# Optimization experiments

Measured on AMD Instinct MI355X. Metric: run time of the kernel, lower is better.

The kernel has to match this reference:

```python
import jax, jax.numpy as jnp
import numpy as np

NBINS = 128
LOGSCALE = False


def setup_inputs() -> dict:
    key = jax.random.key(0)
    X = jax.random.normal(key, (2048, 32768), dtype=jnp.float32)
    return {"X": X}


def reference(X) -> jnp.ndarray:
    # Flatten all non-leading dims (mirrors X.view(len(X), -1))
    X = X.reshape(X.shape[0], -1)
    ns = X.shape[1]
    nfreqs = 2 * (NBINS - 1) + 1          # window length (255)
    hop = nfreqs // 2
    starts = jnp.arange(0, ns - nfreqs + 1, hop)          # [nwin]
    idx = starts[:, None] + jnp.arange(nfreqs)[None, :]    # [nwin, nfreqs]
    W = X[:, idx]                          # [ntrials, nwin, nfreqs] gathered windows
    # One batched rfft + fused |.|^2 and mean over windows (Welch average)
    S = jnp.mean(jnp.abs(jnp.fft.rfft(W, axis=-1)) ** 2, axis=1)  # [ntrials, NBINS]
    if LOGSCALE:
        S = jnp.log10(S)
    return S
```

## Files before the change

kernel.cpp:

```cpp
#include <hip/hip_runtime.h>
#include <hip/hip_bf16.h>

#define NS     32768
#define NROWS  2048
#define HOP    127
#define NW     257
#define NB     128
#define WTILE  16
#define NT     17
#define TWOPI_255 0.02463994236f

typedef _Float16 f16;
typedef __attribute__((ext_vector_type(2))) _Float16 f16x2;
typedef __attribute__((ext_vector_type(8))) _Float16 f16x8;
typedef __attribute__((ext_vector_type(4))) float f32x4;

__device__ inline f32x4 load4u(const float* p) {
    f32x4 v;
    __builtin_memcpy(&v, p, 16);
    return v;
}

__global__ __launch_bounds__(256, 3)
void psd_kernel(const float* __restrict__ X, float* __restrict__ out) {
    const int row  = blockIdx.x;
    const int tid  = threadIdx.x;
    const int lane = tid & 63;
    const int cq   = tid >> 6;
    const int r16  = lane & 15;
    const int kg   = lane >> 4;
    const int is_sin = cq >> 1;

    __shared__ alignas(16) f16 atile[2][WTILE * 256];
    __shared__ float scol[256];

    const float* __restrict__ xrow = X + (size_t)row * NS;

    const int sw  = tid >> 4;
    const int sk0 = (tid & 15) * 8;

    f32x4 fva, fvb, rva, rvb;
    {
        const int b = sw * HOP;
        fva = load4u(xrow + b + sk0);
        fvb = load4u(xrow + b + sk0 + 4);
        rva = load4u(xrow + b + 248 - sk0);
        rvb = load4u(xrow + b + 252 - sk0);
    }

    f16x8 bfrag[4][4];
    #pragma unroll
    for (int nt = 0; nt < 4; ++nt) {
        const int comp = cq * 64 + nt * 16 + r16;
        const int f    = comp & 127;
        #pragma unroll
        for (int kk = 0; kk < 4; ++kk) {
            int m = (f * (kk * 32 + kg * 8)) % 255;
            f16x8 v;
            #pragma unroll
            for (int j = 0; j < 8; ++j) {
                const float ang = (float)m * TWOPI_255;
                const float s   = is_sin ? __sinf(ang) : __cosf(ang);
                v[j] = (f16)s;
                m += f; if (m >= 255) m -= 255;
            }
            bfrag[nt][kk] = v;
        }
    }

    char* const lds = (char*)&atile[0][0];

    const uint swz = (uint)((sw & 7) << 4);
    const uint wr0 = ((uint)(sw * 512 + sk0 * 2)) ^ swz;
    const uint wr1 = ((uint)(sw * 512 + sk0 * 2 + 256)) ^ swz;
    const uint rswz = (uint)((r16 & 7) << 4);
    uint rd[4];
    #pragma unroll
    for (int kk = 0; kk < 4; ++kk)
        rd[kk] = ((uint)(r16 * 512 + is_sin * 256 + kg * 16 + kk * 64)) ^ rswz;

    auto fold_write = [&](char* wp, bool valid) {
        f16x8 h0, h1;
        #pragma unroll
        for (int q = 0; q < 4; ++q) {
            const int j0 = 2 * q, j1 = 2 * q + 1;
            const float f0 = (j0 < 4) ? fva[j0] : fvb[j0 - 4];
            const float f1 = (j1 < 4) ? fva[j1] : fvb[j1 - 4];
            const float r0 = (j0 < 4) ? rvb[3 - j0] : rva[7 - j0];
            const float r1 = (j1 < 4) ? rvb[3 - j1] : rva[7 - j1];
            const f16x2 fp = __builtin_bit_cast(f16x2, __builtin_amdgcn_cvt_pkrtz(f0, f1));
            const f16x2 rp = __builtin_bit_cast(f16x2, __builtin_amdgcn_cvt_pkrtz(r0, r1));
            const f16x2 s = fp + rp;
            const f16x2 d = fp - rp;
            h0[j0] = s[0]; h0[j1] = s[1];
            h1[j0] = d[0]; h1[j1] = d[1];
        }
        if (sk0 == 0) { h0[0] = (f16)fva[0]; h1[0] = (f16)0.0f; }
        if (!valid) {
            #pragma unroll
            for (int j = 0; j < 8; ++j) { h0[j] = (f16)0.0f; h1[j] = (f16)0.0f; }
        }
        *(f16x8*)(wp + wr0) = h0;
        *(f16x8*)(wp + wr1) = h1;
    };

    fold_write(lds, true);
    {
        const int b = (WTILE + sw) * HOP;
        fva = load4u(xrow + b + sk0);
        fvb = load4u(xrow + b + sk0 + 4);
        rva = load4u(xrow + b + 248 - sk0);
        rvb = load4u(xrow + b + 252 - sk0);
    }
    asm volatile("s_waitcnt lgkmcnt(0)" ::: "memory");
    __builtin_amdgcn_s_barrier();
    asm volatile("" ::: "memory");

    f16x8 acur[4], anxt[4];
    #pragma unroll
    for (int kk = 0; kk < 4; ++kk) acur[kk] = *(const f16x8*)(lds + rd[kk]);

    float ssum[4] = {0.f, 0.f, 0.f, 0.f};

    for (int mt = 0; mt < NT; ++mt) {
        if (mt < NT - 1) {
            char* wp = lds + (((mt + 1) & 1) << 13);
            const bool valid = ((mt + 1) * WTILE + sw) < NW;
            fold_write(wp, valid);
            if (mt < NT - 2) {
                const int w = (mt + 2) * WTILE + sw;
                int b = w * HOP; if (b > NS - 256) b = NS - 256;
                fva = load4u(xrow + b + sk0);
                fvb = load4u(xrow + b + sk0 + 4);
                rva = load4u(xrow + b + 248 - sk0);
                rvb = load4u(xrow + b + 252 - sk0);
            }
            asm volatile("s_waitcnt lgkmcnt(0)" ::: "memory");
            __builtin_amdgcn_s_barrier();
            asm volatile("" ::: "memory");
            const char* ap = lds + (((mt + 1) & 1) << 13);
            #pragma unroll
            for (int kk = 0; kk < 4; ++kk)
                anxt[kk] = *(const f16x8*)(ap + rd[kk]);
        }

        f32x4 acc0 = {0,0,0,0}, acc1 = {0,0,0,0}, acc2 = {0,0,0,0}, acc3 = {0,0,0,0};
        __builtin_amdgcn_s_setprio(1);
        #pragma unroll
        for (int kk = 0; kk < 4; ++kk) {
            acc0 = __builtin_amdgcn_mfma_f32_16x16x32_f16(acur[kk], bfrag[0][kk], acc0, 0, 0, 0);
            acc1 = __builtin_amdgcn_mfma_f32_16x16x32_f16(acur[kk], bfrag[1][kk], acc1, 0, 0, 0);
            acc2 = __builtin_amdgcn_mfma_f32_16x16x32_f16(acur[kk], bfrag[2][kk], acc2, 0, 0, 0);
            acc3 = __builtin_amdgcn_mfma_f32_16x16x32_f16(acur[kk], bfrag[3][kk], acc3, 0, 0, 0);
        }
        __builtin_amdgcn_s_setprio(0);
        #pragma unroll
        for (int r = 0; r < 4; ++r) {
            ssum[0] += acc0[r] * acc0[r];
            ssum[1] += acc1[r] * acc1[r];
            ssum[2] += acc2[r] * acc2[r];
            ssum[3] += acc3[r] * acc3[r];
        }

        if (mt < NT - 1) {
            #pragma unroll
            for (int kk = 0; kk < 4; ++kk) acur[kk] = anxt[kk];
        }
    }

    #pragma unroll
    for (int nt = 0; nt < 4; ++nt) {
        float v = ssum[nt];
        v += __shfl_xor(v, 16, 64);
        v += __shfl_xor(v, 32, 64);
        if (kg == 0) scol[cq * 64 + nt * 16 + r16] = v;
    }
    __syncthreads();
    if (tid < NB) {
        out[(size_t)row * NB + tid] = (scol[tid] + scol[tid + NB]) * (1.0f / 257.0f);
    }
}

extern "C" void kernel_launch(void* const* d_in, const int* in_sizes, int n_in,
                              void* d_out, int out_size, void* d_ws, size_t ws_size,
                              hipStream_t stream) {
    const float* X = (const float*)d_in[0];
    float* out = (float*)d_out;
    (void)in_sizes; (void)n_in; (void)d_ws; (void)ws_size; (void)out_size;
    psd_kernel<<<dim3(NROWS), dim3(256), 0, stream>>>(X, out);
}
```

Baseline: 61.83 us.

## Double block size to 512 threads, halving per-thread MFMA and fold work

The block grows from 256 to 512 threads (8 waves), so each wave computes only 2 frequency tiles of 16 instead of 4, and each thread folds 4 samples per window instead of 8. A-fragments are now read from LDS inside the MFMA loop rather than being prefetched into registers for the next tile, and the fold/store of the next tile moves after the compute. Byte-offset addressing with clamped unsigned offsets replaces index arithmetic. The aim is more waves in flight per CU and fewer registers per thread to hide memory latency, at the cost of more LDS traffic per output and less register-level overlap between LDS reads and MFMA.

```diff
diff --git a/kernel.cpp b/kernel.cpp
--- a/kernel.cpp
+++ b/kernel.cpp
@@ -12,16 +12,17 @@
 
 typedef _Float16 f16;
 typedef __attribute__((ext_vector_type(2))) _Float16 f16x2;
+typedef __attribute__((ext_vector_type(4))) _Float16 f16x4;
 typedef __attribute__((ext_vector_type(8))) _Float16 f16x8;
 typedef __attribute__((ext_vector_type(4))) float f32x4;
 
-__device__ inline f32x4 load4u(const float* p) {
+__device__ inline f32x4 load4u(const char* p) {
     f32x4 v;
     __builtin_memcpy(&v, p, 16);
     return v;
 }
 
-__global__ __launch_bounds__(256, 3)
+__global__ __launch_bounds__(512, 6)
 void psd_kernel(const float* __restrict__ X, float* __restrict__ out) {
     const int row  = blockIdx.x;
     const int tid  = threadIdx.x;
@@ -29,30 +30,27 @@
     const int cq   = tid >> 6;
     const int r16  = lane & 15;
     const int kg   = lane >> 4;
-    const int is_sin = cq >> 1;
+    const int is_sin = cq >> 2;
 
     __shared__ alignas(16) f16 atile[2][WTILE * 256];
     __shared__ float scol[256];
 
-    const float* __restrict__ xrow = X + (size_t)row * NS;
+    const char* __restrict__ xrow = (const char*)(X + (size_t)row * NS);
 
-    const int sw  = tid >> 4;
-    const int sk0 = (tid & 15) * 8;
+    const int sw  = tid >> 5;
+    const int sq  = tid & 31;
+    const int sk0 = sq * 4;
 
-    f32x4 fva, fvb, rva, rvb;
-    {
-        const int b = sw * HOP;
-        fva = load4u(xrow + b + sk0);
-        fvb = load4u(xrow + b + sk0 + 4);
-        rva = load4u(xrow + b + 248 - sk0);
-        rvb = load4u(xrow + b + 252 - sk0);
-    }
+    const uint voff_f = (uint)((sw * HOP + sk0) * 4);
+    const uint voff_r = (uint)((sw * HOP + 252 - sk0) * 4);
 
-    f16x8 bfrag[4][4];
+    f32x4 fv = load4u(xrow + voff_f);
+    f32x4 rv = load4u(xrow + voff_r);
+
+    f16x8 bfrag[2][4];
     #pragma unroll
-    for (int nt = 0; nt < 4; ++nt) {
-        const int comp = cq * 64 + nt * 16 + r16;
-        const int f    = comp & 127;
+    for (int nt = 0; nt < 2; ++nt) {
+        const int f = (cq & 3) * 32 + nt * 16 + r16;
         #pragma unroll
         for (int kk = 0; kk < 4; ++kk) {
             int m = (f * (kk * 32 + kg * 8)) % 255;
@@ -60,8 +58,7 @@
             #pragma unroll
             for (int j = 0; j < 8; ++j) {
                 const float ang = (float)m * TWOPI_255;
-                const float s   = is_sin ? __sinf(ang) : __cosf(ang);
-                v[j] = (f16)s;
+                v[j] = (f16)(is_sin ? __sinf(ang) : __cosf(ang));
                 m += f; if (m >= 255) m -= 255;
             }
             bfrag[nt][kk] = v;
@@ -70,9 +67,9 @@
 
     char* const lds = (char*)&atile[0][0];
 
-    const uint swz = (uint)((sw & 7) << 4);
-    const uint wr0 = ((uint)(sw * 512 + sk0 * 2)) ^ swz;
-    const uint wr1 = ((uint)(sw * 512 + sk0 * 2 + 256)) ^ swz;
+    const uint swz  = (uint)((sw & 7) << 4);
+    const uint wr_p = ((uint)(sw * 512 + sq * 8)) ^ swz;
+    const uint wr_m = ((uint)(sw * 512 + sq * 8 + 256)) ^ swz;
     const uint rswz = (uint)((r16 & 7) << 4);
     uint rd[4];
     #pragma unroll
@@ -80,100 +77,79 @@
         rd[kk] = ((uint)(r16 * 512 + is_sin * 256 + kg * 16 + kk * 64)) ^ rswz;
 
     auto fold_write = [&](char* wp, bool valid) {
-        f16x8 h0, h1;
-        #pragma unroll
-        for (int q = 0; q < 4; ++q) {
-            const int j0 = 2 * q, j1 = 2 * q + 1;
-            const float f0 = (j0 < 4) ? fva[j0] : fvb[j0 - 4];
-            const float f1 = (j1 < 4) ? fva[j1] : fvb[j1 - 4];
-            const float r0 = (j0 < 4) ? rvb[3 - j0] : rva[7 - j0];
-            const float r1 = (j1 < 4) ? rvb[3 - j1] : rva[7 - j1];
-            const f16x2 fp = __builtin_bit_cast(f16x2, __builtin_amdgcn_cvt_pkrtz(f0, f1));
-            const f16x2 rp = __builtin_bit_cast(f16x2, __builtin_amdgcn_cvt_pkrtz(r0, r1));
-            const f16x2 s = fp + rp;
-            const f16x2 d = fp - rp;
-            h0[j0] = s[0]; h0[j1] = s[1];
-            h1[j0] = d[0]; h1[j1] = d[1];
-        }
-        if (sk0 == 0) { h0[0] = (f16)fva[0]; h1[0] = (f16)0.0f; }
+        const f16x2 fp01 = __builtin_bit_cast(f16x2, __builtin_amdgcn_cvt_pkrtz(fv[0], fv[1]));
+        const f16x2 fp23 = __builtin_bit_cast(f16x2, __builtin_amdgcn_cvt_pkrtz(fv[2], fv[3]));
+        const f16x2 rp01 = __builtin_bit_cast(f16x2, __builtin_amdgcn_cvt_pkrtz(rv[3], rv[2]));
+        const f16x2 rp23 = __builtin_bit_cast(f16x2, __builtin_amdgcn_cvt_pkrtz(rv[1], rv[0]));
+        const f16x2 yp01 = fp01 + rp01, yp23 = fp23 + rp23;
+        const f16x2 ym01 = fp01 - rp01, ym23 = fp23 - rp23;
+        f16x4 h0, h1;
+        h0[0] = yp01[0]; h0[1] = yp01[1]; h0[2] = yp23[0]; h0[3] = yp23[1];
+        h1[0] = ym01[0]; h1[1] = ym01[1]; h1[2] = ym23[0]; h1[3] = ym23[1];
+        if (sq == 0) { h0[0] = (f16)fv[0]; h1[0] = (f16)0.0f; }
         if (!valid) {
             #pragma unroll
-            for (int j = 0; j < 8; ++j) { h0[j] = (f16)0.0f; h1[j] = (f16)0.0f; }
+            for (int j = 0; j < 4; ++j) { h0[j] = (f16)0.0f; h1[j] = (f16)0.0f; }
         }
-        *(f16x8*)(wp + wr0) = h0;
-        *(f16x8*)(wp + wr1) = h1;
+        *(f16x4*)(wp + wr_p) = h0;
+        *(f16x4*)(wp + wr_m) = h1;
     };
 
     fold_write(lds, true);
     {
-        const int b = (WTILE + sw) * HOP;
-        fva = load4u(xrow + b + sk0);
-        fvb = load4u(xrow + b + sk0 + 4);
-        rva = load4u(xrow + b + 248 - sk0);
-        rvb = load4u(xrow + b + 252 - sk0);
+        const uint base = (uint)(WTILE * HOP * 4);
+        fv = load4u(xrow + (voff_f + base));
+        rv = load4u(xrow + (voff_r + base));
     }
     asm volatile("s_waitcnt lgkmcnt(0)" ::: "memory");
     __builtin_amdgcn_s_barrier();
     asm volatile("" ::: "memory");
 
-    f16x8 acur[4], anxt[4];
-    #pragma unroll
-    for (int kk = 0; kk < 4; ++kk) acur[kk] = *(const f16x8*)(lds + rd[kk]);
-
-    float ssum[4] = {0.f, 0.f, 0.f, 0.f};
+    float ssum0 = 0.f, ssum1 = 0.f;
+    const uint vclamp = (uint)((NS - 4) * 4);
 
     for (int mt = 0; mt < NT; ++mt) {
+        const char* ap = lds + ((mt & 1) << 13);
+
+        f32x4 acc0 = {0,0,0,0}, acc1 = {0,0,0,0};
+        __builtin_amdgcn_s_setprio(1);
+        #pragma unroll
+        for (int kk = 0; kk < 4; ++kk) {
+            const f16x8 af = *(const f16x8*)(ap + rd[kk]);
+            acc0 = __builtin_amdgcn_mfma_f32_16x16x32_f16(af, bfrag[0][kk], acc0, 0, 0, 0);
+            acc1 = __builtin_amdgcn_mfma_f32_16x16x32_f16(af, bfrag[1][kk], acc1, 0, 0, 0);
+        }
+        __builtin_amdgcn_s_setprio(0);
+        #pragma unroll
+        for (int r = 0; r < 4; ++r) {
+            ssum0 += acc0[r] * acc0[r];
+            ssum1 += acc1[r] * acc1[r];
+        }
+
         if (mt < NT - 1) {
             char* wp = lds + (((mt + 1) & 1) << 13);
-            const bool valid = ((mt + 1) * WTILE + sw) < NW;
+            const bool valid = (mt != 15) || (sw == 0);
             fold_write(wp, valid);
             if (mt < NT - 2) {
-                const int w = (mt + 2) * WTILE + sw;
-                int b = w * HOP; if (b > NS - 256) b = NS - 256;
-                fva = load4u(xrow + b + sk0);
-                fvb = load4u(xrow + b + sk0 + 4);
-                rva = load4u(xrow + b + 248 - sk0);
-                rvb = load4u(xrow + b + 252 - sk0);
+                const uint base = (uint)((mt + 2) * WTILE * HOP * 4);
+                fv = load4u(xrow + min(voff_f + base, vclamp));
+                rv = load4u(xrow + min(voff_r + base, vclamp));
             }
             asm volatile("s_waitcnt lgkmcnt(0)" ::: "memory");
             __builtin_amdgcn_s_barrier();
             asm volatile("" ::: "memory");
-            const char* ap = lds + (((mt + 1) & 1) << 13);
-            #pragma unroll
-            for (int kk = 0; kk < 4; ++kk)
-                anxt[kk] = *(const f16x8*)(ap + rd[kk]);
-        }
-
-        f32x4 acc0 = {0,0,0,0}, acc1 = {0,0,0,0}, acc2 = {0,0,0,0}, acc3 = {0,0,0,0};
-        __builtin_amdgcn_s_setprio(1);
-        #pragma unroll
-        for (int kk = 0; kk < 4; ++kk) {
-            acc0 = __builtin_amdgcn_mfma_f32_16x16x32_f16(acur[kk], bfrag[0][kk], acc0, 0, 0, 0);
-            acc1 = __builtin_amdgcn_mfma_f32_16x16x32_f16(acur[kk], bfrag[1][kk], acc1, 0, 0, 0);
-            acc2 = __builtin_amdgcn_mfma_f32_16x16x32_f16(acur[kk], bfrag[2][kk], acc2, 0, 0, 0);
-            acc3 = __builtin_amdgcn_mfma_f32_16x16x32_f16(acur[kk], bfrag[3][kk], acc3, 0, 0, 0);
-        }
-        __builtin_amdgcn_s_setprio(0);
-        #pragma unroll
-        for (int r = 0; r < 4; ++r) {
-            ssum[0] += acc0[r] * acc0[r];
-            ssum[1] += acc1[r] * acc1[r];
-            ssum[2] += acc2[r] * acc2[r];
-            ssum[3] += acc3[r] * acc3[r];
-        }
-
-        if (mt < NT - 1) {
-            #pragma unroll
-            for (int kk = 0; kk < 4; ++kk) acur[kk] = anxt[kk];
         }
     }
 
-    #pragma unroll
-    for (int nt = 0; nt < 4; ++nt) {
-        float v = ssum[nt];
+    {
+        float v = ssum0;
         v += __shfl_xor(v, 16, 64);
         v += __shfl_xor(v, 32, 64);
-        if (kg == 0) scol[cq * 64 + nt * 16 + r16] = v;
+        if (kg == 0) scol[is_sin * 128 + (cq & 3) * 32 + r16] = v;
+        float w = ssum1;
+        w += __shfl_xor(w, 16, 64);
+        w += __shfl_xor(w, 32, 64);
+        if (kg == 0) scol[is_sin * 128 + (cq & 3) * 32 + 16 + r16] = w;
     }
     __syncthreads();
     if (tid < NB) {
@@ -187,5 +163,5 @@
     const float* X = (const float*)d_in[0];
     float* out = (float*)d_out;
     (void)in_sizes; (void)n_in; (void)d_ws; (void)ws_size; (void)out_size;
-    psd_kernel<<<dim3(NROWS), dim3(256), 0, stream>>>(X, out);
+    psd_kernel<<<dim3(NROWS), dim3(512), 0, stream>>>(X, out);
 }
```

New measurement: 60.57 us. 2.0% less time.
